# Optimization experiments

Hardware: AMD Instinct MI355X
Metric: run time of the kernel (lower is better)

Reference implementation:

```python
import jax, jax.numpy as jnp
import numpy as np
from jax import lax

L = 16       # int(log2(input_size)) dilated conv layers
C = 256      # channels (output_size in the torch module)
T = 65536    # input_size; T = 2**L so the stack reduces time to exactly 1


def setup_inputs() -> dict:
    key = jax.random.key(0)
    kx, kw, kb = jax.random.split(key, 3)
    x = jax.random.normal(kx, (1, C, T), dtype=jnp.float32)
    # Conv1d(256, 256, kernel_size=2) weights per layer, OIW layout; scaled ~1/sqrt(fan_in=512)
    W = jax.random.normal(kw, (L, C, C, 2), dtype=jnp.float32) * 0.044
    b = jax.random.normal(kb, (L, C), dtype=jnp.float32) * 0.01
    return {"x": x, "W": W, "b": b}


def reference(x, W, b):
    # Stacked causal dilated convs: layer i uses dilation 2**i, kernel 2, VALID padding,
    # followed by tanh (generation path of the torch module with saves=None).
    for i in range(L):
        y = lax.conv_general_dilated(
            x, W[i],
            window_strides=(1,),
            padding="VALID",
            rhs_dilation=(2 ** i,),
            dimension_numbers=("NCH", "OIH", "NCH"),
        )  # (1, C, T_i - 2**i)
        x = jnp.tanh(y + b[i][None, :, None])
    # final time length is T - (2**L - 1) = 1
    return x.reshape(1, C)
```

## Files before the change

kernel.cpp:

```cpp
#include <hip/hip_runtime.h>
#include <stdint.h>

typedef __attribute__((ext_vector_type(8))) short bhalf8;
typedef __attribute__((ext_vector_type(8))) unsigned short u16x8;
typedef __attribute__((ext_vector_type(4))) float f32x4;

__device__ __forceinline__ unsigned short f2bf(float f) {
  unsigned int u = __float_as_uint(f);
  u += 0x7FFFu + ((u >> 16) & 1u);
  return (unsigned short)(u >> 16);
}

__device__ __forceinline__ void gload16(const void* g, void* l) {
  __builtin_amdgcn_global_load_lds(
      (const __attribute__((address_space(1))) void*)g,
      (__attribute__((address_space(3))) void*)l, 16, 0, 0);
}

__global__ void convert_w_kernel(const float* __restrict__ W,
                                 unsigned short* __restrict__ wbf) {
  int tid = blockIdx.x * 256 + threadIdx.x;
  int k = tid & 511;
  int c = (tid >> 9) & 255;
  int base = tid & ~0x1FFFF;
  int ks = k >> 6;
  int kk = k & 63;
  wbf[base + ks * 16384 + c * 64 + (kk ^ ((c & 7) << 3))] = f2bf(W[tid]);
}

__global__ __launch_bounds__(256, 4)
void layer0_kernel(const float* __restrict__ x0,
                   unsigned short* __restrict__ act0,
                   const unsigned short* __restrict__ w0,
                   const float* __restrict__ bias0) {
  __shared__ __align__(16) unsigned char lds[40960];
  const int tid = threadIdx.x;
  const int lane = tid & 63, w = tid >> 6, l15 = lane & 15, l4 = lane >> 4;
  const long n0 = (long)blockIdx.x * 64;

  f32x4 acc[4][4];
#pragma unroll
  for (int a = 0; a < 4; ++a)
#pragma unroll
    for (int bq = 0; bq < 4; ++bq) acc[a][bq] = (f32x4)0.0f;

  for (int ks = 0; ks < 8; ++ks) {
    const unsigned short* src = w0 + ks * 16384;
#pragma unroll
    for (int rr = 0; rr < 8; ++rr)
      gload16(src + rr * 2048 + tid * 8, lds + rr * 4096 + w * 1024);
#pragma unroll
    for (int p = 0; p < 4; ++p) {
      int idx = p * 256 + tid;
      int cpp = idx >> 5;
      int fch = idx & 31;
      long t = 2 * n0 + 4 * fch;
      const float* row = x0 + ((long)(32 * ks + cpp) << 16);
      f32x4 v = *(const f32x4*)(row + t);
      unsigned int lo = (unsigned)f2bf(v[0]) | ((unsigned)f2bf(v[1]) << 16);
      unsigned int hi = (unsigned)f2bf(v[2]) | ((unsigned)f2bf(v[3]) << 16);
      int colb = 4 * cpp;
      int nl = 2 * fch;
      *(unsigned int*)(lds + 32768 + nl * 128 + (colb ^ ((nl & 7) << 4))) = lo;
      nl++;
      *(unsigned int*)(lds + 32768 + nl * 128 + (colb ^ ((nl & 7) << 4))) = hi;
    }
    __syncthreads();
#pragma unroll
    for (int k2 = 0; k2 < 2; ++k2) {
      int colbase = k2 * 64 + 16 * l4;
      bhalf8 af[4], bfv[4];
#pragma unroll
      for (int mt = 0; mt < 4; ++mt) {
        int m = 64 * w + 16 * mt + l15;
        af[mt] = *(const bhalf8*)(lds + m * 128 + (colbase ^ ((m & 7) << 4)));
      }
#pragma unroll
      for (int nt = 0; nt < 4; ++nt) {
        int n = 16 * nt + l15;
        bfv[nt] = *(const bhalf8*)(lds + 32768 + n * 128 + (colbase ^ ((n & 7) << 4)));
      }
#pragma unroll
      for (int mt = 0; mt < 4; ++mt)
#pragma unroll
        for (int nt = 0; nt < 4; ++nt)
          acc[mt][nt] = __builtin_amdgcn_mfma_f32_16x16x32_bf16(
              af[mt], bfv[nt], acc[mt][nt], 0, 0, 0);
    }
    __syncthreads();
  }
#pragma unroll
  for (int mt = 0; mt < 4; ++mt) {
    int cb_ = 64 * w + 16 * mt + 4 * l4;
#pragma unroll
    for (int q = 0; q < 4; ++q) {
      int c = cb_ + q;
      float bs = bias0[c];
#pragma unroll
      for (int nt = 0; nt < 4; ++nt) {
        int n = 16 * nt + l15;
        unsigned short v = f2bf(tanhf(acc[mt][nt][q] + bs));
        int r2 = n >> 1;
        *(unsigned short*)(lds + r2 * 1024 +
                           ((4 * c + 2 * (n & 1)) ^ ((r2 & 7) << 4))) = v;
      }
    }
  }
  __syncthreads();
#pragma unroll
  for (int p = 0; p < 8; ++p)
    *(u16x8*)(act0 + (long)blockIdx.x * 16384 + p * 2048 + tid * 8) =
        *(const u16x8*)(lds + p * 4096 + tid * 16);
}

template <int NL, int ROWS_IN, int BN_OUT, int FINAL>
__global__ __launch_bounds__(256, 1)
void tree_kernel(const unsigned short* __restrict__ actin,
                 unsigned short* __restrict__ actout,
                 float* __restrict__ fout,
                 const unsigned short* __restrict__ wbase,
                 const float* __restrict__ biasbase) {
  constexpr int BIN = ROWS_IN * 1024;
  constexpr int AOFF = BIN;
  constexpr int BOFF = BIN + 65536;
  __shared__ __align__(16) unsigned char lds[BIN + 65536 + NL * 1024];
  const int tid = threadIdx.x;
  const int lane = tid & 63, w = tid >> 6, l15 = lane & 15, l4 = lane >> 4;
  const long blk = blockIdx.x;

  {
    const unsigned short* src = actin + blk * (ROWS_IN * 512);
#pragma unroll
    for (int rr = 0; rr < BIN / 4096; ++rr)
      gload16(src + rr * 2048 + w * 512 + lane * 8, lds + rr * 4096 + w * 1024);
#pragma unroll
    for (int cb = 0; cb < NL; ++cb)
      if (w == (cb & 3))
        gload16(biasbase + cb * 256 + lane * 4, lds + BOFF + cb * 1024);
#pragma unroll
    for (int rr = 0; rr < 8; ++rr)
      gload16(wbase + rr * 2048 + w * 512 + lane * 8,
              lds + AOFF + rr * 4096 + w * 1024);
  }

  f32x4 acc[4][4];
#pragma unroll
  for (int a = 0; a < 4; ++a)
#pragma unroll
    for (int bq = 0; bq < 4; ++bq) acc[a][bq] = (f32x4)0.0f;

  constexpr int R = NL * 8;
  int r = 0;
#pragma unroll
  for (int j = 0; j < NL; ++j) {
    const int cols = ROWS_IN >> j;
    const int NT = (cols >= 64) ? 4 : (cols >= 32) ? 2 : 1;
    const int in_off = (j & 1) * (BIN / 2);
    const int out_off = (j & 1) ? 0 : (BIN / 2);
#pragma unroll
    for (int ks = 0; ks < 8; ++ks, ++r) {
      const int rn = r + 1;
      if (rn < R) {
        const unsigned short* aw = wbase + (rn >> 3) * 131072 + (rn & 7) * 16384;
        unsigned char* ad = lds + AOFF + (rn & 1) * 32768;
#pragma unroll
        for (int rr2 = 0; rr2 < 8; ++rr2)
          gload16(aw + rr2 * 2048 + w * 512 + lane * 8,
                  ad + rr2 * 4096 + w * 1024);
        asm volatile("s_waitcnt vmcnt(8)" ::: "memory");
      } else {
        asm volatile("s_waitcnt vmcnt(0)" ::: "memory");
      }
      __builtin_amdgcn_sched_barrier(0);
      __builtin_amdgcn_s_barrier();
      const unsigned char* Ab = lds + AOFF + (r & 1) * 32768;
#pragma unroll
      for (int k2 = 0; k2 < 2; ++k2) {
        const int acol = k2 * 64 + 16 * l4;
        bhalf8 af[4], bfv[4];
#pragma unroll
        for (int mt = 0; mt < 4; ++mt) {
          int m = 64 * w + 16 * mt + l15;
          af[mt] = *(const bhalf8*)(Ab + m * 128 + (acol ^ ((m & 7) << 4)));
        }
        const int bcol = ks * 128 + acol;
#pragma unroll
        for (int nt = 0; nt < 4; ++nt)
          if (nt < NT) {
            int n = 16 * nt + l15;
            bfv[nt] = *(const bhalf8*)(lds + in_off + n * 1024 +
                                       (bcol ^ ((n & 7) << 4)));
          }
#pragma unroll
        for (int mt = 0; mt < 4; ++mt)
#pragma unroll
          for (int nt = 0; nt < 4; ++nt)
            if (nt < NT)
              acc[mt][nt] = __builtin_amdgcn_mfma_f32_16x16x32_bf16(
                  af[mt], bfv[nt], acc[mt][nt], 0, 0, 0);
      }
      if (ks == 7) {
        __builtin_amdgcn_s_barrier();
        if (FINAL && j == NL - 1) {
          if (l15 == 0) {
#pragma unroll
            for (int mt = 0; mt < 4; ++mt)
#pragma unroll
              for (int q = 0; q < 4; ++q) {
                int c = 64 * w + 16 * mt + 4 * l4 + q;
                float bs = *(const float*)(lds + BOFF + j * 1024 + c * 4);
                fout[c] = tanhf(acc[mt][0][q] + bs);
              }
          }
        } else if (j == NL - 1 && BN_OUT == 1) {
          long Rg = blk >> 1;
          int par = (int)(blk & 1);
          if (l15 == 0) {
#pragma unroll
            for (int mt = 0; mt < 4; ++mt)
#pragma unroll
              for (int q = 0; q < 4; ++q) {
                int c = 64 * w + 16 * mt + 4 * l4 + q;
                float bs = *(const float*)(lds + BOFF + j * 1024 + c * 4);
                unsigned short v = f2bf(tanhf(acc[mt][0][q] + bs));
                *(unsigned short*)((unsigned char*)actout + Rg * 1024 +
                                   ((4 * c + 2 * par) ^
                                    ((((int)Rg) & 7) << 4))) = v;
              }
          }
        } else {
#pragma unroll
          for (int mt = 0; mt < 4; ++mt) {
            int cb_ = 64 * w + 16 * mt + 4 * l4;
#pragma unroll
            for (int q = 0; q < 4; ++q) {
              int c = cb_ + q;
              float bs = *(const float*)(lds + BOFF + j * 1024 + c * 4);
#pragma unroll
              for (int nt = 0; nt < 4; ++nt)
                if (nt < NT) {
                  int n = 16 * nt + l15;
                  if (n < cols) {
                    unsigned short v = f2bf(tanhf(acc[mt][nt][q] + bs));
                    int r2 = n >> 1;
                    *(unsigned short*)(lds + out_off + r2 * 1024 +
                                       ((4 * c + 2 * (n & 1)) ^
                                        ((r2 & 7) << 4))) = v;
                  }
                }
            }
          }
          asm volatile("s_waitcnt lgkmcnt(0)" ::: "memory");
        }
#pragma unroll
        for (int a = 0; a < 4; ++a)
#pragma unroll
          for (int bq = 0; bq < 4; ++bq) acc[a][bq] = (f32x4)0.0f;
      }
      __builtin_amdgcn_s_barrier();
    }
  }
  if (!FINAL && BN_OUT >= 2) {
    constexpr int OUTB = (BN_OUT / 2) * 1024;
    const int src_off = ((NL - 1) & 1) ? 0 : (BIN / 2);
    unsigned short* dst = actout + blk * (BN_OUT / 2) * 512;
#pragma unroll
    for (int p = 0; p < OUTB / 4096; ++p)
      *(u16x8*)(dst + p * 2048 + tid * 8) =
          *(const u16x8*)(lds + src_off + p * 4096 + tid * 16);
  }
}

extern "C" void kernel_launch(void* const* d_in, const int* in_sizes, int n_in,
                              void* d_out, int out_size, void* d_ws, size_t ws_size,
                              hipStream_t stream) {
  (void)in_sizes; (void)n_in; (void)out_size; (void)ws_size;
  const float* x = (const float*)d_in[0];
  const float* W = (const float*)d_in[1];
  const float* b = (const float*)d_in[2];
  float* out = (float*)d_out;
  unsigned short* wbf = (unsigned short*)d_ws;
  unsigned short* act0 = (unsigned short*)((char*)d_ws + (4l << 20));
  unsigned short* act2 = (unsigned short*)((char*)d_ws + (20l << 20));
  unsigned short* act7 = (unsigned short*)((char*)d_ws + (24l << 20));
  unsigned short* act12 = (unsigned short*)((char*)d_ws + (24l << 20) + (128l << 10));

  convert_w_kernel<<<dim3(8192), dim3(256), 0, stream>>>(W, wbf);
  layer0_kernel<<<dim3(512), dim3(256), 0, stream>>>(x, act0, wbf, b);
  tree_kernel<2, 64, 32, 0><<<dim3(256), dim3(256), 0, stream>>>(
      act0, act2, nullptr, wbf + 1 * 131072, b + 1 * 256);
  tree_kernel<5, 16, 1, 0><<<dim3(256), dim3(256), 0, stream>>>(
      act2, act7, nullptr, wbf + 3 * 131072, b + 3 * 256);
  tree_kernel<5, 16, 1, 0><<<dim3(8), dim3(256), 0, stream>>>(
      act7, act12, nullptr, wbf + 8 * 131072, b + 8 * 256);
  tree_kernel<3, 4, 1, 1><<<dim3(1), dim3(256), 0, stream>>>(
      act12, nullptr, out, wbf + 13 * 131072, b + 13 * 256);
}
```

Before: 220.2 us.

## Pipeline layer0 loads, triple-buffer tree weights, regroup tree kernels into three launches

Layer0 now double-buffers weight and input tiles, prefetching the next K-slice while the current one runs through MFMA. Tree kernels gain a RING parameter for a three-deep weight prefetch ring, and bias is read straight from global memory instead of being staged in LDS. The later layers are regrouped into three launches (2, 6 and 7 layers) with different block sizes, which removes one launch. The cost is a larger LDS footprint that lowers occupancy, and a longer serial single-block final kernel.

```diff
diff --git a/kernel.cpp b/kernel.cpp
--- a/kernel.cpp
+++ b/kernel.cpp
@@ -15,6 +15,18 @@
   __builtin_amdgcn_global_load_lds(
       (const __attribute__((address_space(1))) void*)g,
       (__attribute__((address_space(3))) void*)l, 16, 0, 0);
+}
+
+template <int N>
+__device__ __forceinline__ void vwait() {
+  if constexpr (N == 0)
+    asm volatile("s_waitcnt vmcnt(0)" ::: "memory");
+  else if constexpr (N == 8)
+    asm volatile("s_waitcnt vmcnt(8)" ::: "memory");
+  else if constexpr (N == 12)
+    asm volatile("s_waitcnt vmcnt(12)" ::: "memory");
+  else
+    asm volatile("s_waitcnt vmcnt(16)" ::: "memory");
 }
 
 __global__ void convert_w_kernel(const float* __restrict__ W,
@@ -28,57 +40,91 @@
   wbf[base + ks * 16384 + c * 64 + (kk ^ ((c & 7) << 3))] = f2bf(W[tid]);
 }
 
-__global__ __launch_bounds__(256, 4)
+__global__ __launch_bounds__(256, 2)
 void layer0_kernel(const float* __restrict__ x0,
                    unsigned short* __restrict__ act0,
                    const unsigned short* __restrict__ w0,
                    const float* __restrict__ bias0) {
-  __shared__ __align__(16) unsigned char lds[40960];
+  __shared__ __align__(16) unsigned char lds[81920];
   const int tid = threadIdx.x;
   const int lane = tid & 63, w = tid >> 6, l15 = lane & 15, l4 = lane >> 4;
   const long n0 = (long)blockIdx.x * 64;
 
+  int cpp[4], fch[4];
+#pragma unroll
+  for (int p = 0; p < 4; ++p) {
+    int idx = p * 256 + tid;
+    cpp[p] = idx >> 5;
+    fch[p] = idx & 31;
+  }
+
+  f32x4 xv[2][4];
+#pragma unroll
+  for (int rr = 0; rr < 8; ++rr)
+    gload16(w0 + rr * 2048 + tid * 8, lds + rr * 4096 + w * 1024);
+#pragma unroll
+  for (int p = 0; p < 4; ++p)
+    xv[0][p] = *(const f32x4*)(x0 + ((long)cpp[p] << 16) + 2 * n0 + 4 * fch[p]);
+
   f32x4 acc[4][4];
 #pragma unroll
   for (int a = 0; a < 4; ++a)
 #pragma unroll
     for (int bq = 0; bq < 4; ++bq) acc[a][bq] = (f32x4)0.0f;
 
-  for (int ks = 0; ks < 8; ++ks) {
-    const unsigned short* src = w0 + ks * 16384;
-#pragma unroll
-    for (int rr = 0; rr < 8; ++rr)
-      gload16(src + rr * 2048 + tid * 8, lds + rr * 4096 + w * 1024);
-#pragma unroll
-    for (int p = 0; p < 4; ++p) {
-      int idx = p * 256 + tid;
-      int cpp = idx >> 5;
-      int fch = idx & 31;
-      long t = 2 * n0 + 4 * fch;
-      const float* row = x0 + ((long)(32 * ks + cpp) << 16);
-      f32x4 v = *(const f32x4*)(row + t);
-      unsigned int lo = (unsigned)f2bf(v[0]) | ((unsigned)f2bf(v[1]) << 16);
-      unsigned int hi = (unsigned)f2bf(v[2]) | ((unsigned)f2bf(v[3]) << 16);
-      int colb = 4 * cpp;
-      int nl = 2 * fch;
-      *(unsigned int*)(lds + 32768 + nl * 128 + (colb ^ ((nl & 7) << 4))) = lo;
-      nl++;
-      *(unsigned int*)(lds + 32768 + nl * 128 + (colb ^ ((nl & 7) << 4))) = hi;
-    }
-    __syncthreads();
+#pragma unroll
+  for (int r = 0; r < 8; ++r) {
+    __builtin_amdgcn_s_barrier();
+    __builtin_amdgcn_sched_barrier(0);
+    if (r + 1 < 8) {
+      const unsigned short* aw = w0 + (r + 1) * 16384;
+      unsigned char* ad = lds + ((r + 1) & 1) * 32768;
+#pragma unroll
+      for (int rr = 0; rr < 8; ++rr)
+        gload16(aw + rr * 2048 + tid * 8, ad + rr * 4096 + w * 1024);
+#pragma unroll
+      for (int p = 0; p < 4; ++p)
+        xv[(r + 1) & 1][p] = *(const f32x4*)(
+            x0 + ((long)(32 * (r + 1) + cpp[p]) << 16) + 2 * n0 + 4 * fch[p]);
+      __builtin_amdgcn_sched_barrier(0);
+      vwait<12>();
+    } else {
+      vwait<0>();
+    }
+    __builtin_amdgcn_sched_barrier(0);
+    {
+      unsigned char* bb = lds + 65536 + (r & 1) * 8192;
+#pragma unroll
+      for (int p = 0; p < 4; ++p) {
+        f32x4 v = xv[r & 1][p];
+        unsigned int lo = (unsigned)f2bf(v[0]) | ((unsigned)f2bf(v[1]) << 16);
+        unsigned int hi = (unsigned)f2bf(v[2]) | ((unsigned)f2bf(v[3]) << 16);
+        int colb = 4 * cpp[p];
+        int nl = 2 * fch[p];
+        *(unsigned int*)(bb + nl * 128 + (colb ^ ((nl & 7) << 4))) = lo;
+        nl++;
+        *(unsigned int*)(bb + nl * 128 + (colb ^ ((nl & 7) << 4))) = hi;
+      }
+    }
+    asm volatile("s_waitcnt lgkmcnt(0)" ::: "memory");
+    __builtin_amdgcn_sched_barrier(0);
+    __builtin_amdgcn_s_barrier();
+    __builtin_amdgcn_sched_barrier(0);
+    const unsigned char* Ab = lds + (r & 1) * 32768;
+    const unsigned char* Bb = lds + 65536 + (r & 1) * 8192;
 #pragma unroll
     for (int k2 = 0; k2 < 2; ++k2) {
-      int colbase = k2 * 64 + 16 * l4;
+      const int acol = k2 * 64 + 16 * l4;
       bhalf8 af[4], bfv[4];
 #pragma unroll
       for (int mt = 0; mt < 4; ++mt) {
         int m = 64 * w + 16 * mt + l15;
-        af[mt] = *(const bhalf8*)(lds + m * 128 + (colbase ^ ((m & 7) << 4)));
+        af[mt] = *(const bhalf8*)(Ab + m * 128 + (acol ^ ((m & 7) << 4)));
       }
 #pragma unroll
       for (int nt = 0; nt < 4; ++nt) {
         int n = 16 * nt + l15;
-        bfv[nt] = *(const bhalf8*)(lds + 32768 + n * 128 + (colbase ^ ((n & 7) << 4)));
+        bfv[nt] = *(const bhalf8*)(Bb + n * 128 + (acol ^ ((n & 7) << 4)));
       }
 #pragma unroll
       for (int mt = 0; mt < 4; ++mt)
@@ -87,19 +133,18 @@
           acc[mt][nt] = __builtin_amdgcn_mfma_f32_16x16x32_bf16(
               af[mt], bfv[nt], acc[mt][nt], 0, 0, 0);
     }
-    __syncthreads();
   }
 #pragma unroll
   for (int mt = 0; mt < 4; ++mt) {
     int cb_ = 64 * w + 16 * mt + 4 * l4;
+    f32x4 bs4 = *(const f32x4*)(bias0 + cb_);
 #pragma unroll
     for (int q = 0; q < 4; ++q) {
       int c = cb_ + q;
-      float bs = bias0[c];
 #pragma unroll
       for (int nt = 0; nt < 4; ++nt) {
         int n = 16 * nt + l15;
-        unsigned short v = f2bf(tanhf(acc[mt][nt][q] + bs));
+        unsigned short v = f2bf(tanhf(acc[mt][nt][q] + bs4[q]));
         int r2 = n >> 1;
         *(unsigned short*)(lds + r2 * 1024 +
                            ((4 * c + 2 * (n & 1)) ^ ((r2 & 7) << 4))) = v;
@@ -113,7 +158,7 @@
         *(const u16x8*)(lds + p * 4096 + tid * 16);
 }
 
-template <int NL, int ROWS_IN, int BN_OUT, int FINAL>
+template <int NL, int ROWS_IN, int BN_OUT, int FINAL, int RING>
 __global__ __launch_bounds__(256, 1)
 void tree_kernel(const unsigned short* __restrict__ actin,
                  unsigned short* __restrict__ actout,
@@ -122,25 +167,27 @@
                  const float* __restrict__ biasbase) {
   constexpr int BIN = ROWS_IN * 1024;
   constexpr int AOFF = BIN;
-  constexpr int BOFF = BIN + 65536;
-  __shared__ __align__(16) unsigned char lds[BIN + 65536 + NL * 1024];
+  __shared__ __align__(16) unsigned char lds[BIN + RING * 32768];
   const int tid = threadIdx.x;
   const int lane = tid & 63, w = tid >> 6, l15 = lane & 15, l4 = lane >> 4;
   const long blk = blockIdx.x;
+  constexpr int R = NL * 8;
 
   {
     const unsigned short* src = actin + blk * (ROWS_IN * 512);
 #pragma unroll
     for (int rr = 0; rr < BIN / 4096; ++rr)
       gload16(src + rr * 2048 + w * 512 + lane * 8, lds + rr * 4096 + w * 1024);
-#pragma unroll
-    for (int cb = 0; cb < NL; ++cb)
-      if (w == (cb & 3))
-        gload16(biasbase + cb * 256 + lane * 4, lds + BOFF + cb * 1024);
 #pragma unroll
     for (int rr = 0; rr < 8; ++rr)
       gload16(wbase + rr * 2048 + w * 512 + lane * 8,
               lds + AOFF + rr * 4096 + w * 1024);
+    if (RING == 3) {
+#pragma unroll
+      for (int rr = 0; rr < 8; ++rr)
+        gload16(wbase + 16384 + rr * 2048 + w * 512 + lane * 8,
+                lds + AOFF + 32768 + rr * 4096 + w * 1024);
+    }
   }
 
   f32x4 acc[4][4];
@@ -149,8 +196,6 @@
 #pragma unroll
     for (int bq = 0; bq < 4; ++bq) acc[a][bq] = (f32x4)0.0f;
 
-  constexpr int R = NL * 8;
-  int r = 0;
 #pragma unroll
   for (int j = 0; j < NL; ++j) {
     const int cols = ROWS_IN >> j;
@@ -158,22 +203,47 @@
     const int in_off = (j & 1) * (BIN / 2);
     const int out_off = (j & 1) ? 0 : (BIN / 2);
 #pragma unroll
-    for (int ks = 0; ks < 8; ++ks, ++r) {
-      const int rn = r + 1;
-      if (rn < R) {
-        const unsigned short* aw = wbase + (rn >> 3) * 131072 + (rn & 7) * 16384;
-        unsigned char* ad = lds + AOFF + (rn & 1) * 32768;
-#pragma unroll
-        for (int rr2 = 0; rr2 < 8; ++rr2)
-          gload16(aw + rr2 * 2048 + w * 512 + lane * 8,
-                  ad + rr2 * 4096 + w * 1024);
-        asm volatile("s_waitcnt vmcnt(8)" ::: "memory");
+    for (int ks = 0; ks < 8; ++ks) {
+      const int r = j * 8 + ks;
+      __builtin_amdgcn_s_barrier();
+      __builtin_amdgcn_sched_barrier(0);
+      if (RING == 3) {
+        const int rn = r + 2;
+        if (rn < R) {
+          const unsigned short* aw =
+              wbase + (rn >> 3) * 131072 + (rn & 7) * 16384;
+          unsigned char* ad = lds + AOFF + (rn % 3) * 32768;
+#pragma unroll
+          for (int rr2 = 0; rr2 < 8; ++rr2)
+            gload16(aw + rr2 * 2048 + w * 512 + lane * 8,
+                    ad + rr2 * 4096 + w * 1024);
+          __builtin_amdgcn_sched_barrier(0);
+          vwait<16>();
+        } else if (rn == R) {
+          vwait<8>();
+        } else {
+          vwait<0>();
+        }
       } else {
-        asm volatile("s_waitcnt vmcnt(0)" ::: "memory");
+        const int rn = r + 1;
+        if (rn < R) {
+          const unsigned short* aw =
+              wbase + (rn >> 3) * 131072 + (rn & 7) * 16384;
+          unsigned char* ad = lds + AOFF + (rn & 1) * 32768;
+#pragma unroll
+          for (int rr2 = 0; rr2 < 8; ++rr2)
+            gload16(aw + rr2 * 2048 + w * 512 + lane * 8,
+                    ad + rr2 * 4096 + w * 1024);
+          __builtin_amdgcn_sched_barrier(0);
+          vwait<8>();
+        } else {
+          vwait<0>();
+        }
       }
       __builtin_amdgcn_sched_barrier(0);
       __builtin_amdgcn_s_barrier();
-      const unsigned char* Ab = lds + AOFF + (r & 1) * 32768;
+      __builtin_amdgcn_sched_barrier(0);
+      const unsigned char* Ab = lds + AOFF + (r % RING) * 32768;
 #pragma unroll
       for (int k2 = 0; k2 < 2; ++k2) {
         const int acol = k2 * 64 + 16 * l4;
@@ -201,47 +271,50 @@
       }
       if (ks == 7) {
         __builtin_amdgcn_s_barrier();
+        __builtin_amdgcn_sched_barrier(0);
         if (FINAL && j == NL - 1) {
           if (l15 == 0) {
 #pragma unroll
-            for (int mt = 0; mt < 4; ++mt)
-#pragma unroll
-              for (int q = 0; q < 4; ++q) {
-                int c = 64 * w + 16 * mt + 4 * l4 + q;
-                float bs = *(const float*)(lds + BOFF + j * 1024 + c * 4);
-                fout[c] = tanhf(acc[mt][0][q] + bs);
-              }
+            for (int mt = 0; mt < 4; ++mt) {
+              int cb_ = 64 * w + 16 * mt + 4 * l4;
+              f32x4 bs4 = *(const f32x4*)(biasbase + j * 256 + cb_);
+#pragma unroll
+              for (int q = 0; q < 4; ++q)
+                fout[cb_ + q] = tanhf(acc[mt][0][q] + bs4[q]);
+            }
           }
         } else if (j == NL - 1 && BN_OUT == 1) {
           long Rg = blk >> 1;
           int par = (int)(blk & 1);
           if (l15 == 0) {
 #pragma unroll
-            for (int mt = 0; mt < 4; ++mt)
+            for (int mt = 0; mt < 4; ++mt) {
+              int cb_ = 64 * w + 16 * mt + 4 * l4;
+              f32x4 bs4 = *(const f32x4*)(biasbase + j * 256 + cb_);
 #pragma unroll
               for (int q = 0; q < 4; ++q) {
-                int c = 64 * w + 16 * mt + 4 * l4 + q;
-                float bs = *(const float*)(lds + BOFF + j * 1024 + c * 4);
-                unsigned short v = f2bf(tanhf(acc[mt][0][q] + bs));
+                int c = cb_ + q;
+                unsigned short v = f2bf(tanhf(acc[mt][0][q] + bs4[q]));
                 *(unsigned short*)((unsigned char*)actout + Rg * 1024 +
                                    ((4 * c + 2 * par) ^
                                     ((((int)Rg) & 7) << 4))) = v;
               }
+            }
           }
         } else {
 #pragma unroll
           for (int mt = 0; mt < 4; ++mt) {
             int cb_ = 64 * w + 16 * mt + 4 * l4;
+            f32x4 bs4 = *(const f32x4*)(biasbase + j * 256 + cb_);
 #pragma unroll
             for (int q = 0; q < 4; ++q) {
               int c = cb_ + q;
-              float bs = *(const float*)(lds + BOFF + j * 1024 + c * 4);
 #pragma unroll
               for (int nt = 0; nt < 4; ++nt)
                 if (nt < NT) {
                   int n = 16 * nt + l15;
                   if (n < cols) {
-                    unsigned short v = f2bf(tanhf(acc[mt][nt][q] + bs));
+                    unsigned short v = f2bf(tanhf(acc[mt][nt][q] + bs4[q]));
                     int r2 = n >> 1;
                     *(unsigned short*)(lds + out_off + r2 * 1024 +
                                        ((4 * c + 2 * (n & 1)) ^
@@ -251,16 +324,17 @@
             }
           }
           asm volatile("s_waitcnt lgkmcnt(0)" ::: "memory");
+          __builtin_amdgcn_sched_barrier(0);
         }
 #pragma unroll
         for (int a = 0; a < 4; ++a)
 #pragma unroll
           for (int bq = 0; bq < 4; ++bq) acc[a][bq] = (f32x4)0.0f;
       }
-      __builtin_amdgcn_s_barrier();
     }
   }
   if (!FINAL && BN_OUT >= 2) {
+    __syncthreads();
     constexpr int OUTB = (BN_OUT / 2) * 1024;
     const int src_off = ((NL - 1) & 1) ? 0 : (BIN / 2);
     unsigned short* dst = actout + blk * (BN_OUT / 2) * 512;
@@ -282,17 +356,14 @@
   unsigned short* wbf = (unsigned short*)d_ws;
   unsigned short* act0 = (unsigned short*)((char*)d_ws + (4l << 20));
   unsigned short* act2 = (unsigned short*)((char*)d_ws + (20l << 20));
-  unsigned short* act7 = (unsigned short*)((char*)d_ws + (24l << 20));
-  unsigned short* act12 = (unsigned short*)((char*)d_ws + (24l << 20) + (128l << 10));
+  unsigned short* act9 = (unsigned short*)((char*)d_ws + (24l << 20));
 
   convert_w_kernel<<<dim3(8192), dim3(256), 0, stream>>>(W, wbf);
   layer0_kernel<<<dim3(512), dim3(256), 0, stream>>>(x, act0, wbf, b);
-  tree_kernel<2, 64, 32, 0><<<dim3(256), dim3(256), 0, stream>>>(
+  tree_kernel<2, 32, 16, 0, 3><<<dim3(512), dim3(256), 0, stream>>>(
       act0, act2, nullptr, wbf + 1 * 131072, b + 1 * 256);
-  tree_kernel<5, 16, 1, 0><<<dim3(256), dim3(256), 0, stream>>>(
-      act2, act7, nullptr, wbf + 3 * 131072, b + 3 * 256);
-  tree_kernel<5, 16, 1, 0><<<dim3(8), dim3(256), 0, stream>>>(
-      act7, act12, nullptr, wbf + 8 * 131072, b + 8 * 256);
-  tree_kernel<3, 4, 1, 1><<<dim3(1), dim3(256), 0, stream>>>(
-      act12, nullptr, out, wbf + 13 * 131072, b + 13 * 256);
-}
+  tree_kernel<6, 32, 1, 0, 3><<<dim3(128), dim3(256), 0, stream>>>(
+      act2, act9, nullptr, wbf + 3 * 131072, b + 3 * 256);
+  tree_kernel<7, 64, 1, 1, 2><<<dim3(1), dim3(256), 0, stream>>>(
+      act9, nullptr, out, wbf + 9 * 131072, b + 9 * 256);
+}
```

After: 236.3 us. 7.3% more time.
